# Kernel tuning notes

Measured on AMD Instinct MI355X. Metric: run time of the kernel, lower is better.

## Reference

```python
import jax, jax.numpy as jnp
import numpy as np

TEMPERATURE = 0.07


def setup_inputs() -> dict:
    key = jax.random.key(0)
    k1, k2 = jax.random.split(key)
    B, D = 8192, 256
    embeddings = jax.random.normal(k1, (B, D), dtype=jnp.float32)
    ids = jax.random.randint(k2, (B,), 0, 1024, dtype=jnp.int64 if jax.config.jax_enable_x64 else jnp.int32)
    return {"embeddings": embeddings, "ids": ids}


def reference(embeddings, ids):
    B = embeddings.shape[0]
    # L2-normalize rows (F.normalize with p=2, dim=1)
    emb = embeddings / jnp.maximum(jnp.linalg.norm(embeddings, axis=1, keepdims=True), 1e-12)
    sim = (emb @ emb.T) / TEMPERATURE                      # [B, B]
    eye = jnp.eye(B, dtype=bool)
    sim = jnp.where(eye, -jnp.inf, sim)
    exp_sim = jnp.exp(sim)                                  # diag -> 0
    pos_mask = (ids[:, None] == ids[None, :]) & ~eye        # [B, B]
    pos_sum = jnp.sum(jnp.where(pos_mask, exp_sim, 0.0), axis=1)  # [B]
    all_sum = jnp.sum(exp_sim, axis=1)                      # [B]
    valid = pos_mask.any(axis=1)
    per_row = -jnp.log(pos_sum / all_sum)
    loss = jnp.sum(jnp.where(valid, per_row, 0.0))
    n_valid = jnp.sum(valid.astype(jnp.float32))
    return loss / jnp.maximum(n_valid, 1.0)
```

## Files before the change

### kernel.cpp

```cpp
#include <hip/hip_runtime.h>
#include <hip/hip_bf16.h>
#include <hip/hip_fp8.h>

#define B_SZ 8192
#define D_SZ 256
#define NTILES 2080
#define GRID_SIM 512
#define PRESCALE 4.539816004686735f

#define WAIT_VM8 0x0F78
#define WAIT_VM0 0x0F70

typedef __attribute__((ext_vector_type(4))) float f32x4;

__device__ __forceinline__ void async_copy16(const void* g, void* l) {
    __builtin_amdgcn_global_load_lds(
        (const __attribute__((address_space(1))) unsigned int*)g,
        (__attribute__((address_space(3))) unsigned int*)l,
        16, 0, 0);
}

__global__ __launch_bounds__(256) void norm_kernel(const float* __restrict__ emb,
                                                   unsigned char* __restrict__ nq,
                                                   float* __restrict__ sums) {
    sums[blockIdx.x * 64 + (threadIdx.x >> 2)] = 0.0f;

    const int wave = threadIdx.x >> 6, lane = threadIdx.x & 63;
    for (int g = blockIdx.x; g < B_SZ / 4; g += 256) {
        const int row = g * 4 + wave;
        const float4 v = ((const float4*)(emb + (size_t)row * D_SZ))[lane];
        float ss = v.x * v.x + v.y * v.y + v.z * v.z + v.w * v.w;
        #pragma unroll
        for (int m = 1; m < 64; m <<= 1) ss += __shfl_xor(ss, m, 64);
        float s = PRESCALE / fmaxf(sqrtf(ss), 1e-12f);
        __hip_fp8_e4m3 q0(v.x * s), q1(v.y * s), q2(v.z * s), q3(v.w * s);
        uchar4 o;
        o.x = q0.__x; o.y = q1.__x; o.z = q2.__x; o.w = q3.__x;
        ((uchar4*)(nq + (size_t)row * D_SZ))[lane] = o;
    }
}

__device__ __forceinline__ void decode_tile(int tb, int& i0, int& j0, bool& diag) {
    int bj = (int)((sqrtf(8.0f * tb + 1.0f) - 1.0f) * 0.5f);
    while ((bj + 1) * (bj + 2) / 2 <= tb) ++bj;
    while (bj * (bj + 1) / 2 > tb) --bj;
    const int bi = tb - bj * (bj + 1) / 2;
    i0 = bi * 128; j0 = bj * 128; diag = (bi == bj);
}

__device__ __forceinline__ void issue_panel(const unsigned char* __restrict__ src,
                                            unsigned char* dst, int k0, int lane) {
    const int rowIn = lane >> 2;
    const int slot  = lane & 3;
    #pragma unroll
    for (int q = 0; q < 4; ++q) {
        const int rl  = q * 16 + rowIn;
        const int c16 = slot ^ ((rl >> 1) & 3);
        async_copy16(src + (size_t)rl * D_SZ + k0 + c16 * 16, dst + q * 1024);
    }
}

__device__ __forceinline__ void compute_stage(const unsigned char* sAb,
                                              const unsigned char* sBb,
                                              f32x4 acc[4][4], int lane) {
    #pragma unroll
    for (int ks = 0; ks < 2; ++ks) {
        const int C8 = ks * 4 + (lane >> 4);
        const int hi = C8 >> 1, lo = (C8 & 1) * 8;
        long long af[4], bf[4];
        #pragma unroll
        for (int mi = 0; mi < 4; ++mi) {
            const int rl = mi * 16 + (lane & 15);
            const int s16 = hi ^ ((rl >> 1) & 3);
            af[mi] = *(const long long*)&sAb[rl * 64 + s16 * 16 + lo];
        }
        #pragma unroll
        for (int ni = 0; ni < 4; ++ni) {
            const int rl = ni * 16 + (lane & 15);
            const int s16 = hi ^ ((rl >> 1) & 3);
            bf[ni] = *(const long long*)&sBb[rl * 64 + s16 * 16 + lo];
        }
        #pragma unroll
        for (int mi = 0; mi < 4; ++mi)
            #pragma unroll
            for (int ni = 0; ni < 4; ++ni)
                acc[mi][ni] = __builtin_amdgcn_mfma_f32_16x16x32_fp8_fp8(
                    af[mi], bf[ni], acc[mi][ni], 0, 0, 0);
    }
}

__global__ __launch_bounds__(256) void sim_kernel(const unsigned char* __restrict__ N,
                                                  const int* __restrict__ ids,
                                                  float* __restrict__ all_sum,
                                                  float* __restrict__ pos_sum) {
    __shared__ __align__(16) unsigned char smem[65536];

    const int t    = threadIdx.x;
    const int wave = t >> 6, lane = t & 63;
    const int wy   = wave >> 1, wx = wave & 1;
    const int myc  = lane & 15;
    unsigned char* lds = smem + wave * 16384;

    int tb = blockIdx.x;
    int i0, j0; bool diag;
    decode_tile(tb, i0, j0, diag);
    const unsigned char* gA = N + (size_t)(i0 + wy * 64) * D_SZ;
    const unsigned char* gB = N + (size_t)(j0 + wx * 64) * D_SZ;

    issue_panel(gA, lds, 0, lane);
    issue_panel(gB, lds + 4096, 0, lane);

    while (true) {
        const int ntb = tb + GRID_SIM;
        const bool have_next = (ntb < NTILES);
        int ni0 = i0, nj0 = j0; bool ndiag = diag;
        if (have_next) decode_tile(ntb, ni0, nj0, ndiag);
        const unsigned char* ngA = N + (size_t)(ni0 + wy * 64) * D_SZ;
        const unsigned char* ngB = N + (size_t)(nj0 + wx * 64) * D_SZ;

        f32x4 acc[4][4];
        #pragma unroll
        for (int mi = 0; mi < 4; ++mi)
            #pragma unroll
            for (int ni = 0; ni < 4; ++ni)
                acc[mi][ni] = (f32x4){0.f, 0.f, 0.f, 0.f};

        #pragma unroll
        for (int kk = 0; kk < 4; ++kk) {
            unsigned char* cur = lds + (kk & 1) * 8192;
            unsigned char* nxt = lds + ((kk + 1) & 1) * 8192;
            if (kk < 3) {
                issue_panel(gA, nxt, (kk + 1) * 64, lane);
                issue_panel(gB, nxt + 4096, (kk + 1) * 64, lane);
                __builtin_amdgcn_s_waitcnt(WAIT_VM8);
            } else if (have_next) {
                issue_panel(ngA, nxt, 0, lane);
                issue_panel(ngB, nxt + 4096, 0, lane);
                __builtin_amdgcn_s_waitcnt(WAIT_VM8);
            } else {
                __builtin_amdgcn_s_waitcnt(WAIT_VM0);
            }
            compute_stage(cur, cur + 4096, acc, lane);
        }

        const int R0 = i0 + wy * 64;
        const int C0 = j0 + wx * 64;
        int idc[4];
        #pragma unroll
        for (int ni = 0; ni < 4; ++ni)
            idc[ni] = ids[C0 + ni * 16 + myc];

        float cAll[4] = {0.f, 0.f, 0.f, 0.f};
        float cPos[4] = {0.f, 0.f, 0.f, 0.f};

        #pragma unroll
        for (int mi = 0; mi < 4; ++mi) {
            const int rb = mi * 16 + (lane >> 4) * 4;
            const int4 idr = *(const int4*)&ids[R0 + rb];
            float rAll[4] = {0.f, 0.f, 0.f, 0.f};
            float rPos[4] = {0.f, 0.f, 0.f, 0.f};
            #pragma unroll
            for (int ni = 0; ni < 4; ++ni) {
                #pragma unroll
                for (int rg = 0; rg < 4; ++rg) {
                    float e = __builtin_amdgcn_exp2f(acc[mi][ni][rg]);
                    if (diag && wy == wx && (rb + rg) == (ni * 16 + myc)) e = 0.0f;
                    rAll[rg] += e; cAll[ni] += e;
                    const int idrv = (rg == 0) ? idr.x : (rg == 1) ? idr.y
                                   : (rg == 2) ? idr.z : idr.w;
                    if (idrv == idc[ni]) { rPos[rg] += e; cPos[ni] += e; }
                }
            }
            #pragma unroll
            for (int rg = 0; rg < 4; ++rg) {
                #pragma unroll
                for (int mm = 1; mm < 16; mm <<= 1) {
                    rAll[rg] += __shfl_xor(rAll[rg], mm, 64);
                    rPos[rg] += __shfl_xor(rPos[rg], mm, 64);
                }
            }
            if (myc == 0) {
                #pragma unroll
                for (int rg = 0; rg < 4; ++rg) {
                    atomicAdd(&all_sum[R0 + rb + rg], rAll[rg]);
                    if (rPos[rg] != 0.0f) atomicAdd(&pos_sum[R0 + rb + rg], rPos[rg]);
                }
            }
        }

        if (!diag) {
            #pragma unroll
            for (int ni = 0; ni < 4; ++ni) {
                cAll[ni] += __shfl_xor(cAll[ni], 16, 64);
                cAll[ni] += __shfl_xor(cAll[ni], 32, 64);
                cPos[ni] += __shfl_xor(cPos[ni], 16, 64);
                cPos[ni] += __shfl_xor(cPos[ni], 32, 64);
            }
            if (lane < 16) {
                #pragma unroll
                for (int ni = 0; ni < 4; ++ni) {
                    atomicAdd(&all_sum[C0 + ni * 16 + lane], cAll[ni]);
                    if (cPos[ni] != 0.0f) atomicAdd(&pos_sum[C0 + ni * 16 + lane], cPos[ni]);
                }
            }
        }

        if (!have_next) break;
        tb = ntb; i0 = ni0; j0 = nj0; diag = ndiag; gA = ngA; gB = ngB;
    }
}

__global__ __launch_bounds__(256) void loss_kernel(const float* __restrict__ all_sum,
                                                   const float* __restrict__ pos_sum,
                                                   float* __restrict__ out) {
    float loss = 0.0f, cnt = 0.0f;
    for (int i = threadIdx.x; i < B_SZ; i += 256) {
        float p = pos_sum[i], a = all_sum[i];
        if (p > 0.0f) { loss += logf(a) - logf(p); cnt += 1.0f; }
    }
    #pragma unroll
    for (int m = 1; m < 64; m <<= 1) {
        loss += __shfl_xor(loss, m, 64);
        cnt  += __shfl_xor(cnt, m, 64);
    }
    __shared__ float sl[4], sc[4];
    int wave = threadIdx.x >> 6, lane = threadIdx.x & 63;
    if (lane == 0) { sl[wave] = loss; sc[wave] = cnt; }
    __syncthreads();
    if (threadIdx.x == 0) {
        float L = sl[0] + sl[1] + sl[2] + sl[3];
        float C = sc[0] + sc[1] + sc[2] + sc[3];
        out[0] = L / fmaxf(C, 1.0f);
    }
}

extern "C" void kernel_launch(void* const* d_in, const int* in_sizes, int n_in,
                              void* d_out, int out_size, void* d_ws, size_t ws_size,
                              hipStream_t stream) {
    const float* emb = (const float*)d_in[0];
    const int*   ids = (const int*)d_in[1];
    float*       out = (float*)d_out;

    float*         all_sum = (float*)d_ws;
    float*         pos_sum = all_sum + B_SZ;
    unsigned char* nq      = (unsigned char*)d_ws + 65536;

    norm_kernel<<<256, 256, 0, stream>>>(emb, nq, all_sum);
    sim_kernel<<<GRID_SIM, 256, 0, stream>>>(nq, ids, all_sum, pos_sum);
    loss_kernel<<<1, 256, 0, stream>>>(all_sum, pos_sum, out);
}
```

Baseline: 123.7 us.

## Load full-K operand fragments straight into registers, dropping LDS staging

Replaces the LDS double-buffered async global-to-LDS pipeline with direct global loads of the whole 64x256 fp8 A and B panels into registers (64 long longs per lane). The loads for the next tile are issued after the MFMA chain, so they overlap the exp/reduction epilogue. This removes LDS traffic and waitcnt stalls, but raises register pressure considerably. It also issues uncoalesced 8-byte strided global loads that depend on L2 reuse, since each panel is re-read by several waves.

```diff
diff --git a/kernel.cpp b/kernel.cpp
--- a/kernel.cpp
+++ b/kernel.cpp
@@ -8,17 +8,7 @@
 #define GRID_SIM 512
 #define PRESCALE 4.539816004686735f
 
-#define WAIT_VM8 0x0F78
-#define WAIT_VM0 0x0F70
-
 typedef __attribute__((ext_vector_type(4))) float f32x4;
-
-__device__ __forceinline__ void async_copy16(const void* g, void* l) {
-    __builtin_amdgcn_global_load_lds(
-        (const __attribute__((address_space(1))) unsigned int*)g,
-        (__attribute__((address_space(3))) unsigned int*)l,
-        16, 0, 0);
-}
 
 __global__ __launch_bounds__(256) void norm_kernel(const float* __restrict__ emb,
                                                    unsigned char* __restrict__ nq,
@@ -48,44 +38,17 @@
     i0 = bi * 128; j0 = bj * 128; diag = (bi == bj);
 }
 
-__device__ __forceinline__ void issue_panel(const unsigned char* __restrict__ src,
-                                            unsigned char* dst, int k0, int lane) {
-    const int rowIn = lane >> 2;
-    const int slot  = lane & 3;
+__device__ __forceinline__ void load_frags(long long frag[4][8],
+                                           const unsigned char* __restrict__ base,
+                                           int lane) {
+    const int lr = lane & 15;
+    const int q8 = (lane >> 4) * 8;
     #pragma unroll
-    for (int q = 0; q < 4; ++q) {
-        const int rl  = q * 16 + rowIn;
-        const int c16 = slot ^ ((rl >> 1) & 3);
-        async_copy16(src + (size_t)rl * D_SZ + k0 + c16 * 16, dst + q * 1024);
-    }
-}
-
-__device__ __forceinline__ void compute_stage(const unsigned char* sAb,
-                                              const unsigned char* sBb,
-                                              f32x4 acc[4][4], int lane) {
-    #pragma unroll
-    for (int ks = 0; ks < 2; ++ks) {
-        const int C8 = ks * 4 + (lane >> 4);
-        const int hi = C8 >> 1, lo = (C8 & 1) * 8;
-        long long af[4], bf[4];
-        #pragma unroll
-        for (int mi = 0; mi < 4; ++mi) {
-            const int rl = mi * 16 + (lane & 15);
-            const int s16 = hi ^ ((rl >> 1) & 3);
-            af[mi] = *(const long long*)&sAb[rl * 64 + s16 * 16 + lo];
-        }
-        #pragma unroll
-        for (int ni = 0; ni < 4; ++ni) {
-            const int rl = ni * 16 + (lane & 15);
-            const int s16 = hi ^ ((rl >> 1) & 3);
-            bf[ni] = *(const long long*)&sBb[rl * 64 + s16 * 16 + lo];
-        }
-        #pragma unroll
-        for (int mi = 0; mi < 4; ++mi)
-            #pragma unroll
-            for (int ni = 0; ni < 4; ++ni)
-                acc[mi][ni] = __builtin_amdgcn_mfma_f32_16x16x32_fp8_fp8(
-                    af[mi], bf[ni], acc[mi][ni], 0, 0, 0);
+    for (int f = 0; f < 4; ++f) {
+        const unsigned char* rp = base + (size_t)(f * 16 + lr) * D_SZ + q8;
+        #pragma unroll
+        for (int kb = 0; kb < 8; ++kb)
+            frag[f][kb] = *(const long long*)(rp + kb * 32);
     }
 }
 
@@ -93,58 +56,49 @@
                                                   const int* __restrict__ ids,
                                                   float* __restrict__ all_sum,
                                                   float* __restrict__ pos_sum) {
-    __shared__ __align__(16) unsigned char smem[65536];
-
     const int t    = threadIdx.x;
     const int wave = t >> 6, lane = t & 63;
     const int wy   = wave >> 1, wx = wave & 1;
     const int myc  = lane & 15;
-    unsigned char* lds = smem + wave * 16384;
 
     int tb = blockIdx.x;
     int i0, j0; bool diag;
     decode_tile(tb, i0, j0, diag);
-    const unsigned char* gA = N + (size_t)(i0 + wy * 64) * D_SZ;
-    const unsigned char* gB = N + (size_t)(j0 + wx * 64) * D_SZ;
-
-    issue_panel(gA, lds, 0, lane);
-    issue_panel(gB, lds + 4096, 0, lane);
+
+    long long a_frag[4][8], b_frag[4][8];
+    load_frags(a_frag, N + (size_t)(i0 + wy * 64) * D_SZ, lane);
+    load_frags(b_frag, N + (size_t)(j0 + wx * 64) * D_SZ, lane);
 
     while (true) {
+        const int R0 = i0 + wy * 64;
+        const int C0 = j0 + wx * 64;
+        const bool d_quad = diag && (wy == wx);
+
+        f32x4 acc[4][4];
+        #pragma unroll
+        for (int mi = 0; mi < 4; ++mi)
+            #pragma unroll
+            for (int ni = 0; ni < 4; ++ni)
+                acc[mi][ni] = (f32x4){0.f, 0.f, 0.f, 0.f};
+
+        #pragma unroll
+        for (int kb = 0; kb < 8; ++kb)
+            #pragma unroll
+            for (int mi = 0; mi < 4; ++mi)
+                #pragma unroll
+                for (int ni = 0; ni < 4; ++ni)
+                    acc[mi][ni] = __builtin_amdgcn_mfma_f32_16x16x32_fp8_fp8(
+                        a_frag[mi][kb], b_frag[ni][kb], acc[mi][ni], 0, 0, 0);
+
         const int ntb = tb + GRID_SIM;
         const bool have_next = (ntb < NTILES);
         int ni0 = i0, nj0 = j0; bool ndiag = diag;
-        if (have_next) decode_tile(ntb, ni0, nj0, ndiag);
-        const unsigned char* ngA = N + (size_t)(ni0 + wy * 64) * D_SZ;
-        const unsigned char* ngB = N + (size_t)(nj0 + wx * 64) * D_SZ;
-
-        f32x4 acc[4][4];
-        #pragma unroll
-        for (int mi = 0; mi < 4; ++mi)
-            #pragma unroll
-            for (int ni = 0; ni < 4; ++ni)
-                acc[mi][ni] = (f32x4){0.f, 0.f, 0.f, 0.f};
-
-        #pragma unroll
-        for (int kk = 0; kk < 4; ++kk) {
-            unsigned char* cur = lds + (kk & 1) * 8192;
-            unsigned char* nxt = lds + ((kk + 1) & 1) * 8192;
-            if (kk < 3) {
-                issue_panel(gA, nxt, (kk + 1) * 64, lane);
-                issue_panel(gB, nxt + 4096, (kk + 1) * 64, lane);
-                __builtin_amdgcn_s_waitcnt(WAIT_VM8);
-            } else if (have_next) {
-                issue_panel(ngA, nxt, 0, lane);
-                issue_panel(ngB, nxt + 4096, 0, lane);
-                __builtin_amdgcn_s_waitcnt(WAIT_VM8);
-            } else {
-                __builtin_amdgcn_s_waitcnt(WAIT_VM0);
-            }
-            compute_stage(cur, cur + 4096, acc, lane);
+        if (have_next) {
+            decode_tile(ntb, ni0, nj0, ndiag);
+            load_frags(a_frag, N + (size_t)(ni0 + wy * 64) * D_SZ, lane);
+            load_frags(b_frag, N + (size_t)(nj0 + wx * 64) * D_SZ, lane);
         }
 
-        const int R0 = i0 + wy * 64;
-        const int C0 = j0 + wx * 64;
         int idc[4];
         #pragma unroll
         for (int ni = 0; ni < 4; ++ni)
@@ -164,7 +118,7 @@
                 #pragma unroll
                 for (int rg = 0; rg < 4; ++rg) {
                     float e = __builtin_amdgcn_exp2f(acc[mi][ni][rg]);
-                    if (diag && wy == wx && (rb + rg) == (ni * 16 + myc)) e = 0.0f;
+                    if (d_quad && (rb + rg) == (ni * 16 + myc)) e = 0.0f;
                     rAll[rg] += e; cAll[ni] += e;
                     const int idrv = (rg == 0) ? idr.x : (rg == 1) ? idr.y
                                    : (rg == 2) ? idr.z : idr.w;
@@ -206,7 +160,7 @@
         }
 
         if (!have_next) break;
-        tb = ntb; i0 = ni0; j0 = nj0; diag = ndiag; gA = ngA; gB = ngB;
+        tb = ntb; i0 = ni0; j0 = nj0; diag = ndiag;
     }
 }
 
```

After: 192.9 us. +55.9%, slower.
